# Kernel optimization log

Hardware: AMD Instinct MI355X
Metric: run time of the kernel (lower is better)

Reference implementation:

```python
import jax, jax.numpy as jnp
import numpy as np

NUM_HEADS = 16
HEAD_DIM = 64
PATCH_NUMS = [1, 2, 3, 4, 5, 6, 8, 10, 13, 16, 32]
MAX_SCALE_MUL = float(np.log(100.0))


def precompute_freqs_cis(dim, patch_nums, theta=10000.0):
    # Returns [L, dim//2, 2] (cos, sin) pairs; matches torch.polar construction.
    freqs = 1.0 / theta ** (np.arange(0, dim, 4)[: dim // 4].astype(np.float32) / dim)  # [dim//4]
    tx, ty = [], []
    grid = 32.0
    for p in patch_nums:
        ix, iy = np.meshgrid(np.arange(p), np.arange(p), indexing="ij")  # torch default 'ij'
        tx.append(ix.flatten().astype(np.float32) / p * grid)
        ty.append(iy.flatten().astype(np.float32) / p * grid)
    tx = np.concatenate(tx)
    ty = np.concatenate(ty)
    ang = np.concatenate([np.outer(tx, freqs), np.outer(ty, freqs)], axis=1).astype(np.float32)  # [L, dim//2]
    return np.stack([np.cos(ang), np.sin(ang)], axis=-1)  # [L, dim//2, 2]


FREQS_CIS_CROSS = jnp.asarray(precompute_freqs_cis(HEAD_DIM, [12]))  # [144, 32, 2]


def _rope(x, cis):
    # x: [B, H, S, D]; cis: [S, D//2, 2] -> complex multiply on (even, odd) pairs.
    B, H, S, D = x.shape
    xr = x.reshape(B, H, S, D // 2, 2)
    a, b = xr[..., 0], xr[..., 1]
    c = cis[..., 0][None, None]  # [1,1,S,D//2]
    d = cis[..., 1][None, None]
    return jnp.stack([a * c - b * d, a * d + b * c], axis=-1).reshape(B, H, S, D)


def setup_inputs() -> dict:
    key = jax.random.key(0)
    ks = jax.random.split(key, 6)
    B, C, Ck, Lk = 8, 1024, 1024, 144
    fc = precompute_freqs_cis(HEAD_DIM, PATCH_NUMS)
    L = fc.shape[0]  # 1704
    return {
        "x": jax.random.normal(ks[0], (B, L, C), jnp.float32),
        "y": jax.random.normal(ks[1], (B, Lk, Ck), jnp.float32),
        "freqs_cis": jnp.asarray(fc),
        "attn_bias": jax.random.normal(ks[2], (1, 1, L, Lk), jnp.float32) * 0.1,
        "Wq": jax.random.normal(ks[3], (C, C), jnp.float32) * 0.02,
        "q_bias": jnp.zeros((C,), jnp.float32),
        "Wkv": jax.random.normal(ks[4], (2 * C, Ck), jnp.float32) * 0.02,
        "v_bias": jnp.zeros((C,), jnp.float32),
        "Wproj": jax.random.normal(ks[5], (C, C), jnp.float32) * 0.02,
        "b_proj": jnp.zeros((C,), jnp.float32),
        "scale_mul": jnp.full((1, NUM_HEADS, 1, 1), np.log(4.0), jnp.float32),
    }


def reference(x, y, freqs_cis, attn_bias, Wq, q_bias, Wkv, v_bias, Wproj, b_proj, scale_mul):
    B, L, C = x.shape
    H, D = NUM_HEADS, HEAD_DIM
    Lk = y.shape[1]
    # fused QKV projections (k bias is the zero buffer)
    q = (x @ Wq.T + q_bias).reshape(B, L, H, D).transpose(0, 2, 1, 3)  # [B,H,L,D]
    kv_bias = jnp.concatenate([jnp.zeros_like(v_bias), v_bias])
    kv = (y @ Wkv.T + kv_bias).reshape(B, Lk, 2, H, D)
    k = kv[:, :, 0].transpose(0, 2, 1, 3)  # [B,H,Lk,D]
    v = kv[:, :, 1].transpose(0, 2, 1, 3)
    # attn_l2_norm path: scale = 1, per-head learned multiplier
    sm = jnp.exp(jnp.minimum(scale_mul, MAX_SCALE_MUL))  # [1,H,1,1]
    q = q / jnp.maximum(jnp.linalg.norm(q, axis=-1, keepdims=True), 1e-12) * sm
    k = k / jnp.maximum(jnp.linalg.norm(k, axis=-1, keepdims=True), 1e-12)
    # inline RoPE (cross freqs recomputed from 12x12 grid every forward in the original)
    q = _rope(q, freqs_cis)
    k = _rope(k, FREQS_CIS_CROSS)
    # manual (non-flash) masked attention, scale = 1 due to l2 norm
    logits = jnp.einsum("bhld,bhkd->bhlk", q, k) + attn_bias
    attn = jax.nn.softmax(logits, axis=-1)
    oup = jnp.einsum("bhlk,bhkd->bhld", attn, v).transpose(0, 2, 1, 3).reshape(B, L, C)
    return oup @ Wproj.T + b_proj
```

## Files before the change

kernel.cpp:

```cpp
#include <hip/hip_runtime.h>

using u16 = unsigned short;
using u32 = unsigned int;

typedef __bf16 bf16x8 __attribute__((ext_vector_type(8)));
typedef float  f32x4  __attribute__((ext_vector_type(4)));
typedef _Float16 f16;
typedef _Float16 f16x4 __attribute__((ext_vector_type(4)));
typedef _Float16 f16x8 __attribute__((ext_vector_type(8)));
typedef u16 u16x4 __attribute__((ext_vector_type(4)));

__device__ __forceinline__ float b2f(u16 u) { return __uint_as_float(((u32)u) << 16); }
__device__ __forceinline__ u16 f2b(float f) {
    u32 u = __float_as_uint(f);
    return (u16)((u + 0x7FFFu + ((u >> 16) & 1u)) >> 16);
}

__device__ __forceinline__ void async_cp16(void* lds, const void* g) {
    __builtin_amdgcn_global_load_lds(
        (const __attribute__((address_space(1))) u32*)g,
        (__attribute__((address_space(3))) u32*)lds, 16, 0, 0);
}

__device__ __forceinline__ void split4_store(const float* src, u16* hi, u16* lo, int i) {
    f32x4 v = reinterpret_cast<const f32x4*>(src)[i];
    u16x4 H, L;
#pragma unroll
    for (int j = 0; j < 4; j++) {
        u16 hb = f2b(v[j]);
        H[j] = hb;
        L[j] = f2b(v[j] - b2f(hb));
    }
    reinterpret_cast<u16x4*>(hi)[i] = H;
    reinterpret_cast<u16x4*>(lo)[i] = L;
}

__global__ __launch_bounds__(256) void prep(const float* __restrict__ x,
                                            const float* __restrict__ Wq,
                                            const float* __restrict__ Wp,
                                            u16* __restrict__ xhi, u16* __restrict__ xlo,
                                            u16* __restrict__ wqhi, u16* __restrict__ wqlo,
                                            f16* __restrict__ wph,
                                            int nx4, int nw4) {
    int i = blockIdx.x * 256 + threadIdx.x;
    if (i < nx4) {
        split4_store(x, xhi, xlo, i);
    } else if (i < nx4 + nw4) {
        split4_store(Wq, wqhi, wqlo, i - nx4);
    } else {
        int k = i - nx4 - nw4;
        if (k < nw4) {
            f32x4 v = reinterpret_cast<const f32x4*>(Wp)[k];
            f16x4 h = {(f16)v[0], (f16)v[1], (f16)v[2], (f16)v[3]};
            reinterpret_cast<f16x4*>(wph)[k] = h;
        }
    }
}

__device__ __forceinline__ void split8(f32x4 a0, f32x4 a1, bf16x8& hi, bf16x8& lo) {
    union { bf16x8 v; u16 s[8]; } H, L;
#pragma unroll
    for (int j = 0; j < 4; j++) {
        float f = a0[j]; u16 hb = f2b(f); H.s[j] = hb;     L.s[j] = f2b(f - b2f(hb));
        float g = a1[j]; u16 gb = f2b(g); H.s[4 + j] = gb; L.s[4 + j] = f2b(g - b2f(gb));
    }
    hi = H.v; lo = L.v;
}

__device__ __forceinline__ void remap852(int j, int& mt, int& sg) {
    if (j < 832) {
        int a = j >> 5, rem = j & 31;
        mt = a * 8 + (rem & 7);
        sg = rem >> 3;
    } else {
        int rem = j - 832;
        mt = 208 + rem % 5;
        sg = rem / 5;
    }
}

__global__ __launch_bounds__(256) void gemm_q(const u16* __restrict__ xhi,
                                              const u16* __restrict__ xlo,
                                              const u16* __restrict__ whi,
                                              const u16* __restrict__ wlo,
                                              const float* __restrict__ qb,
                                              const float* __restrict__ fc,
                                              const float* __restrict__ smul,
                                              f16* __restrict__ qout) {
    const int K = 1024, L = 1704;
    __shared__ u16 xs[2][2][64][64];
    int tid = threadIdx.x;
    int lane = tid & 63, wv = tid >> 6;
    int mt, hg;
    remap852(blockIdx.x, mt, hg);
    int h  = hg * 4 + wv;
    int lr = lane & 15, quad = lane >> 4;
    long m0 = (long)mt * 64;

    int r0 = tid >> 3, c0 = tid & 7;
    int s1 = tid + 256;
    int r1 = s1 >> 3, c1 = s1 & 7;
    const u16* srch0 = xhi + (m0 + r0) * K + ((c0 ^ (r0 & 7)) * 8);
    const u16* srch1 = xhi + (m0 + r1) * K + ((c1 ^ (r1 & 7)) * 8);
    const u16* srcl0 = xlo + (m0 + r0) * K + ((c0 ^ (r0 & 7)) * 8);
    const u16* srcl1 = xlo + (m0 + r1) * K + ((c1 ^ (r1 & 7)) * 8);
    u16* dh[2][2]; u16* dl[2][2];
    dh[0][0] = &xs[0][0][r0][c0 * 8]; dh[0][1] = &xs[0][0][r1][c1 * 8];
    dh[1][0] = &xs[1][0][r0][c0 * 8]; dh[1][1] = &xs[1][0][r1][c1 * 8];
    dl[0][0] = &xs[0][1][r0][c0 * 8]; dl[0][1] = &xs[0][1][r1][c1 * 8];
    dl[1][0] = &xs[1][1][r0][c0 * 8]; dl[1][1] = &xs[1][1][r1][c1 * 8];

    const bf16x8* wh_p[4];
    const bf16x8* wl_p[4];
#pragma unroll
    for (int i = 0; i < 4; i++) {
        long woff = ((long)(h * 64 + i * 16 + lr)) * K;
        wh_p[i] = reinterpret_cast<const bf16x8*>(whi + woff) + quad;
        wl_p[i] = reinterpret_cast<const bf16x8*>(wlo + woff) + quad;
    }

    int sp0 = ((0 + quad) ^ (lr & 7)) * 8;
    int sp1 = ((4 + quad) ^ (lr & 7)) * 8;

    f32x4 acc[4][4] = {};

    async_cp16(dh[0][0], srch0); async_cp16(dh[0][1], srch1);
    async_cp16(dl[0][0], srcl0); async_cp16(dl[0][1], srcl1);
    __syncthreads();

    for (int c = 0; c < 16; c++) {
        if (c < 15) {
            int nb = (c + 1) & 1;
            int off = (c + 1) * 64;
            async_cp16(dh[nb][0], srch0 + off); async_cp16(dh[nb][1], srch1 + off);
            async_cp16(dl[nb][0], srcl0 + off); async_cp16(dl[nb][1], srcl1 + off);
        }
        int buf = c & 1;
#pragma unroll
        for (int s = 0; s < 2; s++) {
            int sp = s ? sp1 : sp0;
            bf16x8 AH[4], AL[4], WH[4], WL[4];
#pragma unroll
            for (int i = 0; i < 4; i++) {
                WH[i] = wh_p[i][c * 8 + s * 4];
                WL[i] = wl_p[i][c * 8 + s * 4];
            }
#pragma unroll
            for (int i = 0; i < 4; i++) {
                AH[i] = *reinterpret_cast<const bf16x8*>(&xs[buf][0][i * 16 + lr][sp]);
                AL[i] = *reinterpret_cast<const bf16x8*>(&xs[buf][1][i * 16 + lr][sp]);
            }
#pragma unroll
            for (int mi = 0; mi < 4; mi++)
#pragma unroll
                for (int ni = 0; ni < 4; ni++) {
                    acc[mi][ni] = __builtin_amdgcn_mfma_f32_16x16x32_bf16(AH[mi], WH[ni], acc[mi][ni], 0, 0, 0);
                    acc[mi][ni] = __builtin_amdgcn_mfma_f32_16x16x32_bf16(AL[mi], WH[ni], acc[mi][ni], 0, 0, 0);
                    acc[mi][ni] = __builtin_amdgcn_mfma_f32_16x16x32_bf16(AH[mi], WL[ni], acc[mi][ni], 0, 0, 0);
                }
        }
        __syncthreads();
    }

    float sm = __expf(fminf(smul[h], 4.6051702f));
#pragma unroll
    for (int mi = 0; mi < 4; mi++) {
#pragma unroll
        for (int r = 0; r < 4; r++) {
            long rowg = m0 + mi * 16 + quad * 4 + r;
            float v[4];
            float ss = 0.f;
#pragma unroll
            for (int ni = 0; ni < 4; ni++) {
                v[ni] = acc[mi][ni][r] + qb[h * 64 + ni * 16 + lr];
                ss += v[ni] * v[ni];
            }
            ss += __shfl_xor(ss, 1, 64); ss += __shfl_xor(ss, 2, 64);
            ss += __shfl_xor(ss, 4, 64); ss += __shfl_xor(ss, 8, 64);
            float inv = sm / fmaxf(sqrtf(ss), 1e-12f);
            int l = (int)(rowg % L);
            f16* orow = qout + rowg * 1024 + h * 64;
#pragma unroll
            for (int ni = 0; ni < 4; ni++) {
                float u = v[ni] * inv;
                int d = ni * 16 + lr;
                int j = d >> 1;
                float c = fc[(l * 32 + j) * 2];
                float s = fc[(l * 32 + j) * 2 + 1];
                float pr = __shfl_xor(u, 1, 64);
                float o = (lane & 1) ? (pr * s + u * c) : (u * c - pr * s);
                orow[d] = (f16)o;
            }
        }
    }
}

__constant__ double FREQS16[16] = {
    1.0, 0.5623413251903491, 0.31622776601683794, 0.17782794100389228,
    0.1, 0.05623413251903491, 0.03162277660168379, 0.017782794100389228,
    0.01, 0.005623413251903491, 0.0031622776601683794, 0.0017782794100389228,
    0.001, 0.0005623413251903491, 0.00031622776601683794, 0.00017782794100389228};

__global__ __launch_bounds__(256) void gemm_kv(const float* __restrict__ y,
                                               const float* __restrict__ Wkv,
                                               const float* __restrict__ vb,
                                               f16* __restrict__ khp,
                                               f16* __restrict__ klp,
                                               f16* __restrict__ vhp,
                                               f16* __restrict__ vlp) {
    const int K = 1024;
    int lane = threadIdx.x & 63, wv = threadIdx.x >> 6;
    int mt = blockIdx.x >> 3;
    int nt = (blockIdx.x & 7) * 4 + wv;
    int lr = lane & 15, quad = lane >> 4;
    long m0 = (long)mt * 64;

    const float* arow[4];
    const float* wrow[4];
#pragma unroll
    for (int i = 0; i < 4; i++) {
        arow[i] = y   + (m0 + i * 16 + lr) * K + quad * 8;
        wrow[i] = Wkv + ((long)(nt * 64 + i * 16 + lr)) * K + quad * 8;
    }

    f32x4 acc[4][4] = {};
    for (int ks = 0; ks < 32; ks++) {
        bf16x8 ah[4], al[4], wh[4], wl[4];
#pragma unroll
        for (int i = 0; i < 4; i++) {
            const float* ap = arow[i] + ks * 32;
            split8(*(const f32x4*)ap, *(const f32x4*)(ap + 4), ah[i], al[i]);
            const float* wp = wrow[i] + ks * 32;
            split8(*(const f32x4*)wp, *(const f32x4*)(wp + 4), wh[i], wl[i]);
        }
#pragma unroll
        for (int mi = 0; mi < 4; mi++)
#pragma unroll
            for (int ni = 0; ni < 4; ni++) {
                acc[mi][ni] = __builtin_amdgcn_mfma_f32_16x16x32_bf16(ah[mi], wh[ni], acc[mi][ni], 0, 0, 0);
                acc[mi][ni] = __builtin_amdgcn_mfma_f32_16x16x32_bf16(al[mi], wh[ni], acc[mi][ni], 0, 0, 0);
                acc[mi][ni] = __builtin_amdgcn_mfma_f32_16x16x32_bf16(ah[mi], wl[ni], acc[mi][ni], 0, 0, 0);
            }
    }

    bool isv = nt >= 16;
    int h = isv ? nt - 16 : nt;
#pragma unroll
    for (int mi = 0; mi < 4; mi++) {
#pragma unroll
        for (int r = 0; r < 4; r++) {
            long row = m0 + mi * 16 + quad * 4 + r;
            int b = (int)(row / 144), lk = (int)(row % 144);
            long bh = b * 16 + h;
            float v[4];
#pragma unroll
            for (int ni = 0; ni < 4; ni++)
                v[ni] = acc[mi][ni][r] + (isv ? vb[h * 64 + ni * 16 + lr] : 0.f);
            if (!isv) {
                float ss = v[0] * v[0] + v[1] * v[1] + v[2] * v[2] + v[3] * v[3];
                ss += __shfl_xor(ss, 1, 64); ss += __shfl_xor(ss, 2, 64);
                ss += __shfl_xor(ss, 4, 64); ss += __shfl_xor(ss, 8, 64);
                float inv = 1.f / fmaxf(sqrtf(ss), 1e-12f);
                f16* kh_row = khp + (bh * 144 + lk) * 64;
                f16* kl_row = klp + (bh * 144 + lk) * 64;
#pragma unroll
                for (int ni = 0; ni < 4; ni++) {
                    float u = v[ni] * inv;
                    int d = ni * 16 + lr;
                    int j = d >> 1;
                    int f = j & 15;
                    float tc = (j < 16) ? ((float)(lk / 12)) / 12.0f * 32.0f
                                        : ((float)(lk % 12)) / 12.0f * 32.0f;
                    float ang = (float)((double)tc * FREQS16[f]);
                    float c = cosf(ang), s = sinf(ang);
                    float pr = __shfl_xor(u, 1, 64);
                    float o = (lane & 1) ? (pr * s + u * c) : (u * c - pr * s);
                    f16 oh = (f16)o;
                    f16 ol = (f16)(o - (float)oh);
                    kh_row[d] = oh;
                    kl_row[d] = ol;
                }
            } else {
#pragma unroll
                for (int ni = 0; ni < 4; ni++) {
                    float val = v[ni];
                    int d = ni * 16 + lr;
                    f16 vh = (f16)val;
                    f16 vl = (f16)(val - (float)vh);
                    vhp[(bh * 64 + d) * 144 + lk] = vh;
                    vlp[(bh * 64 + d) * 144 + lk] = vl;
                }
            }
        }
    }
}

__global__ __launch_bounds__(256, 3) void attn(const f16* q,
                                               const f16* __restrict__ khp,
                                               const f16* __restrict__ klp,
                                               const f16* __restrict__ vhp,
                                               const f16* __restrict__ vlp,
                                               const float* __restrict__ abias,
                                               f16* aout) {
    const int L = 1704;
    __shared__ __align__(16) f16 ps[4][16][152];
    int tid = threadIdx.x;
    int lane = tid & 63, wv = tid >> 6;
    int lr = lane & 15, quad = lane >> 4;
    int ltile = blockIdx.x % 27;
    int bh = blockIdx.x / 27;
    int h = bh & 15, b = bh >> 4;
    int l0 = ltile * 64;
    int rows = min(64, L - l0);

    int rA = wv * 16 + lr;
    int rAc = min(rA, rows - 1);
    const f16* qrow = q + ((long)(b * L + l0 + rAc)) * 1024 + h * 64;
    f16x8 qa0 = *reinterpret_cast<const f16x8*>(qrow + quad * 8);
    f16x8 qa1 = *reinterpret_cast<const f16x8*>(qrow + 32 + quad * 8);

    const f16* khb = khp + (long)bh * (144 * 64);
    const f16* klb = klp + (long)bh * (144 * 64);

    f32x4 acc[9] = {};
#pragma unroll
    for (int t = 0; t < 9; t++) {
        const f16* k0 = khb + (t * 16 + lr) * 64 + quad * 8;
        const f16* k1 = klb + (t * 16 + lr) * 64 + quad * 8;
        f16x8 bh0 = *reinterpret_cast<const f16x8*>(k0);
        f16x8 bh1 = *reinterpret_cast<const f16x8*>(k0 + 32);
        f16x8 bl0 = *reinterpret_cast<const f16x8*>(k1);
        f16x8 bl1 = *reinterpret_cast<const f16x8*>(k1 + 32);
        __builtin_amdgcn_s_setprio(1);
        acc[t] = __builtin_amdgcn_mfma_f32_16x16x32_f16(qa0, bh0, acc[t], 0, 0, 0);
        acc[t] = __builtin_amdgcn_mfma_f32_16x16x32_f16(qa1, bh1, acc[t], 0, 0, 0);
        acc[t] = __builtin_amdgcn_mfma_f32_16x16x32_f16(qa0, bl0, acc[t], 0, 0, 0);
        acc[t] = __builtin_amdgcn_mfma_f32_16x16x32_f16(qa1, bl1, acc[t], 0, 0, 0);
        __builtin_amdgcn_s_setprio(0);
    }

    int rC = wv * 16 + quad * 4;
#pragma unroll
    for (int r = 0; r < 4; r++) {
        long lrow = (long)(l0 + min(rC + r, rows - 1)) * 144;
#pragma unroll
        for (int t = 0; t < 9; t++) acc[t][r] += abias[lrow + t * 16 + lr];
    }

#pragma unroll
    for (int r = 0; r < 4; r++) {
        float mx = acc[0][r];
#pragma unroll
        for (int t = 1; t < 9; t++) mx = fmaxf(mx, acc[t][r]);
        mx = fmaxf(mx, __shfl_xor(mx, 1, 64));
        mx = fmaxf(mx, __shfl_xor(mx, 2, 64));
        mx = fmaxf(mx, __shfl_xor(mx, 4, 64));
        mx = fmaxf(mx, __shfl_xor(mx, 8, 64));
        float s = 0.f;
#pragma unroll
        for (int t = 0; t < 9; t++) {
            float e = __expf(acc[t][r] - mx);
            acc[t][r] = e;
            s += e;
        }
        s += __shfl_xor(s, 1, 64);
        s += __shfl_xor(s, 2, 64);
        s += __shfl_xor(s, 4, 64);
        s += __shfl_xor(s, 8, 64);
        float inv = 1.0f / s;
#pragma unroll
        for (int t = 0; t < 9; t++)
            ps[wv][quad * 4 + r][t * 16 + lr] = (f16)(acc[t][r] * inv);
    }

    const f16* vhb = vhp + (long)bh * (64 * 144);
    const f16* vlb = vlp + (long)bh * (64 * 144);
    f32x4 oacc[4] = {};
#pragma unroll
    for (int ks = 0; ks < 5; ks++) {
        f16x8 pa = {0, 0, 0, 0, 0, 0, 0, 0};
        if (ks < 4 || quad < 2)
            pa = *reinterpret_cast<const f16x8*>(&ps[wv][lr][ks * 32 + quad * 8]);
#pragma unroll
        for (int n = 0; n < 4; n++) {
            f16x8 vh8 = {0, 0, 0, 0, 0, 0, 0, 0};
            f16x8 vl8 = {0, 0, 0, 0, 0, 0, 0, 0};
            if (ks < 4 || quad < 2) {
                const f16* vr  = vhb + (n * 16 + lr) * 144 + ks * 32 + quad * 8;
                const f16* vr2 = vlb + (n * 16 + lr) * 144 + ks * 32 + quad * 8;
                vh8 = *reinterpret_cast<const f16x8*>(vr);
                vl8 = *reinterpret_cast<const f16x8*>(vr2);
            }
            __builtin_amdgcn_s_setprio(1);
            oacc[n] = __builtin_amdgcn_mfma_f32_16x16x32_f16(pa, vh8, oacc[n], 0, 0, 0);
            oacc[n] = __builtin_amdgcn_mfma_f32_16x16x32_f16(pa, vl8, oacc[n], 0, 0, 0);
            __builtin_amdgcn_s_setprio(0);
        }
    }

    long ob = (long)(b * L + l0);
#pragma unroll
    for (int r = 0; r < 4; r++) {
        int rw = rC + r;
        if (rw < rows) {
            f16* ao = aout + (ob + rw) * 1024 + h * 64;
#pragma unroll
            for (int n = 0; n < 4; n++) ao[n * 16 + lr] = (f16)oacc[n][r];
        }
    }
}

__global__ __launch_bounds__(256) void gemm_proj(const f16* __restrict__ A,
                                                 const f16* __restrict__ Wh,
                                                 const float* __restrict__ bias,
                                                 float* __restrict__ out) {
    const int K = 1024;
    __shared__ f16 as[2][64][64];
    int tid = threadIdx.x;
    int lane = tid & 63, wv = tid >> 6;
    int mt, cg;
    remap852(blockIdx.x, mt, cg);
    int lr = lane & 15, quad = lane >> 4;
    long m0 = (long)mt * 64;
    long n0 = (long)cg * 256 + wv * 64;

    int r0 = tid >> 3, c0 = tid & 7;
    int s1i = tid + 256;
    int r1 = s1i >> 3, c1 = s1i & 7;
    const f16* srca0 = A + (m0 + r0) * K + ((c0 ^ (r0 & 7)) * 8);
    const f16* srca1 = A + (m0 + r1) * K + ((c1 ^ (r1 & 7)) * 8);
    f16* da[2][2];
    da[0][0] = &as[0][r0][c0 * 8]; da[0][1] = &as[0][r1][c1 * 8];
    da[1][0] = &as[1][r0][c0 * 8]; da[1][1] = &as[1][r1][c1 * 8];

    const f16x8* wrow[4];
#pragma unroll
    for (int i = 0; i < 4; i++)
        wrow[i] = reinterpret_cast<const f16x8*>(Wh + (n0 + i * 16 + lr) * K) + quad;

    int sp0 = ((0 + quad) ^ (lr & 7)) * 8;
    int sp1 = ((4 + quad) ^ (lr & 7)) * 8;

    f32x4 acc[4][4] = {};

    async_cp16(da[0][0], srca0);
    async_cp16(da[0][1], srca1);
    __syncthreads();

    for (int c = 0; c < 16; c++) {
        if (c < 15) {
            int nb = (c + 1) & 1;
            int off = (c + 1) * 64;
            async_cp16(da[nb][0], srca0 + off);
            async_cp16(da[nb][1], srca1 + off);
        }
        int buf = c & 1;
#pragma unroll
        for (int s = 0; s < 2; s++) {
            int sp = s ? sp1 : sp0;
            f16x8 af[4], wf[4];
#pragma unroll
            for (int i = 0; i < 4; i++) wf[i] = wrow[i][c * 8 + s * 4];
#pragma unroll
            for (int i = 0; i < 4; i++)
                af[i] = *reinterpret_cast<const f16x8*>(&as[buf][i * 16 + lr][sp]);
#pragma unroll
            for (int mi = 0; mi < 4; mi++)
#pragma unroll
                for (int ni = 0; ni < 4; ni++)
                    acc[mi][ni] = __builtin_amdgcn_mfma_f32_16x16x32_f16(af[mi], wf[ni], acc[mi][ni], 0, 0, 0);
        }
        __syncthreads();
    }

#pragma unroll
    for (int ni = 0; ni < 4; ni++) {
        int col = (int)n0 + ni * 16 + lr;
        float b = bias[col];
#pragma unroll
        for (int mi = 0; mi < 4; mi++) {
            long row = m0 + mi * 16 + quad * 4;
#pragma unroll
            for (int r = 0; r < 4; r++)
                out[(row + r) * 1024 + col] = acc[mi][ni][r] + b;
        }
    }
}

extern "C" void kernel_launch(void* const* d_in, const int* in_sizes, int n_in,
                              void* d_out, int out_size, void* d_ws, size_t ws_size,
                              hipStream_t stream) {
    const float* x     = (const float*)d_in[0];
    const float* y     = (const float*)d_in[1];
    const float* fc    = (const float*)d_in[2];
    const float* abias = (const float*)d_in[3];
    const float* Wq    = (const float*)d_in[4];
    const float* qb    = (const float*)d_in[5];
    const float* Wkv   = (const float*)d_in[6];
    const float* vb    = (const float*)d_in[7];
    const float* Wp    = (const float*)d_in[8];
    const float* bp    = (const float*)d_in[9];
    const float* smul  = (const float*)d_in[10];

    const long XN = 13959168L;
    const long WN = 1048576L;
    const long KVN = 1179648L;

    f16* qbuf  = (f16*)d_ws;
    u16* wq_hi = (u16*)(qbuf + XN);
    u16* wq_lo = wq_hi + WN;
    f16* wp_h  = (f16*)(wq_lo + WN);

    u16* x_hi = (u16*)d_out;
    u16* x_lo = x_hi + XN;
    f16* kh_p  = (f16*)d_out;
    f16* kl_p  = kh_p + KVN;
    f16* vth_p = kl_p + KVN;
    f16* vtl_p = vth_p + KVN;

    int nx4 = (int)(XN / 4);
    int nw4 = (int)(WN / 4);
    int prep_blocks = (nx4 + 2 * nw4) / 256;

    prep<<<dim3(prep_blocks), dim3(256), 0, stream>>>(x, Wq, Wp, x_hi, x_lo,
                                                      wq_hi, wq_lo, wp_h, nx4, nw4);
    gemm_q<<<dim3(852), dim3(256), 0, stream>>>(x_hi, x_lo, wq_hi, wq_lo, qb, fc, smul, qbuf);
    gemm_kv<<<dim3(144), dim3(256), 0, stream>>>(y, Wkv, vb, kh_p, kl_p, vth_p, vtl_p);
    attn<<<dim3(3456), dim3(256), 0, stream>>>(qbuf, kh_p, kl_p, vth_p, vtl_p, abias, (f16*)qbuf);
    gemm_proj<<<dim3(852), dim3(256), 0, stream>>>((const f16*)qbuf, wp_h, bp, (float*)d_out);
}
```

Measured before the change: 571.0 us.

## Merge double barriers into one and issue weight loads before the LDS wait

In the Q-projection and output-projection GEMM loops, the two __syncthreads per iteration are replaced by a single s_barrier preceded by a partial vmcnt wait. All weight fragments for the chunk are now issued as global loads before that wait, so their latency overlaps the wait for the async LDS copies. The next chunk's prefetch goes out after the barrier. The vmcnt counts are hand-tuned to the number of outstanding loads and rely on in-order counter retirement, which is fragile if the compiler reorders or adds memory operations, and holding both halves of the weights raises register pressure.

```diff
diff --git a/kernel.cpp b/kernel.cpp
--- a/kernel.cpp
+++ b/kernel.cpp
@@ -126,25 +126,30 @@
 
     async_cp16(dh[0][0], srch0); async_cp16(dh[0][1], srch1);
     async_cp16(dl[0][0], srcl0); async_cp16(dl[0][1], srcl1);
-    __syncthreads();
 
     for (int c = 0; c < 16; c++) {
+        int buf = c & 1;
+        bf16x8 WH[2][4], WL[2][4];
+#pragma unroll
+        for (int s = 0; s < 2; s++)
+#pragma unroll
+            for (int i = 0; i < 4; i++) {
+                WH[s][i] = wh_p[i][c * 8 + s * 4];
+                WL[s][i] = wl_p[i][c * 8 + s * 4];
+            }
+        asm volatile("s_waitcnt vmcnt(16)" ::: "memory");
+        __builtin_amdgcn_s_barrier();
+        __builtin_amdgcn_sched_barrier(0);
         if (c < 15) {
             int nb = (c + 1) & 1;
             int off = (c + 1) * 64;
             async_cp16(dh[nb][0], srch0 + off); async_cp16(dh[nb][1], srch1 + off);
             async_cp16(dl[nb][0], srcl0 + off); async_cp16(dl[nb][1], srcl1 + off);
         }
-        int buf = c & 1;
 #pragma unroll
         for (int s = 0; s < 2; s++) {
             int sp = s ? sp1 : sp0;
-            bf16x8 AH[4], AL[4], WH[4], WL[4];
-#pragma unroll
-            for (int i = 0; i < 4; i++) {
-                WH[i] = wh_p[i][c * 8 + s * 4];
-                WL[i] = wl_p[i][c * 8 + s * 4];
-            }
+            bf16x8 AH[4], AL[4];
 #pragma unroll
             for (int i = 0; i < 4; i++) {
                 AH[i] = *reinterpret_cast<const bf16x8*>(&xs[buf][0][i * 16 + lr][sp]);
@@ -154,12 +159,11 @@
             for (int mi = 0; mi < 4; mi++)
 #pragma unroll
                 for (int ni = 0; ni < 4; ni++) {
-                    acc[mi][ni] = __builtin_amdgcn_mfma_f32_16x16x32_bf16(AH[mi], WH[ni], acc[mi][ni], 0, 0, 0);
-                    acc[mi][ni] = __builtin_amdgcn_mfma_f32_16x16x32_bf16(AL[mi], WH[ni], acc[mi][ni], 0, 0, 0);
-                    acc[mi][ni] = __builtin_amdgcn_mfma_f32_16x16x32_bf16(AH[mi], WL[ni], acc[mi][ni], 0, 0, 0);
+                    acc[mi][ni] = __builtin_amdgcn_mfma_f32_16x16x32_bf16(AH[mi], WH[s][ni], acc[mi][ni], 0, 0, 0);
+                    acc[mi][ni] = __builtin_amdgcn_mfma_f32_16x16x32_bf16(AL[mi], WH[s][ni], acc[mi][ni], 0, 0, 0);
+                    acc[mi][ni] = __builtin_amdgcn_mfma_f32_16x16x32_bf16(AH[mi], WL[s][ni], acc[mi][ni], 0, 0, 0);
                 }
         }
-        __syncthreads();
     }
 
     float sm = __expf(fminf(smul[h], 4.6051702f));
@@ -445,22 +449,27 @@
 
     async_cp16(da[0][0], srca0);
     async_cp16(da[0][1], srca1);
-    __syncthreads();
 
     for (int c = 0; c < 16; c++) {
+        int buf = c & 1;
+        f16x8 wf[2][4];
+#pragma unroll
+        for (int s = 0; s < 2; s++)
+#pragma unroll
+            for (int i = 0; i < 4; i++) wf[s][i] = wrow[i][c * 8 + s * 4];
+        asm volatile("s_waitcnt vmcnt(8)" ::: "memory");
+        __builtin_amdgcn_s_barrier();
+        __builtin_amdgcn_sched_barrier(0);
         if (c < 15) {
             int nb = (c + 1) & 1;
             int off = (c + 1) * 64;
             async_cp16(da[nb][0], srca0 + off);
             async_cp16(da[nb][1], srca1 + off);
         }
-        int buf = c & 1;
 #pragma unroll
         for (int s = 0; s < 2; s++) {
             int sp = s ? sp1 : sp0;
-            f16x8 af[4], wf[4];
-#pragma unroll
-            for (int i = 0; i < 4; i++) wf[i] = wrow[i][c * 8 + s * 4];
+            f16x8 af[4];
 #pragma unroll
             for (int i = 0; i < 4; i++)
                 af[i] = *reinterpret_cast<const f16x8*>(&as[buf][i * 16 + lr][sp]);
@@ -468,9 +477,8 @@
             for (int mi = 0; mi < 4; mi++)
 #pragma unroll
                 for (int ni = 0; ni < 4; ni++)
-                    acc[mi][ni] = __builtin_amdgcn_mfma_f32_16x16x32_f16(af[mi], wf[ni], acc[mi][ni], 0, 0, 0);
-        }
-        __syncthreads();
+                    acc[mi][ni] = __builtin_amdgcn_mfma_f32_16x16x32_f16(af[mi], wf[s][ni], acc[mi][ni], 0, 0, 0);
+        }
     }
 
 #pragma unroll
```

Measured after the change: 637.2 us. +11.6%, slower.
